# Kernel optimization log

Measured on AMD Instinct MI355X. Metric: run time of the kernel, lower is better.

## Reference

```python
import jax, jax.numpy as jnp
import numpy as np

N_NODES = 50000
N_EDGES = 800000
D_IN = 128
HIDDEN = 128
NUM_GRAPHS = 64
NUM_CLASSES = 6


def setup_inputs() -> dict:
    key = jax.random.key(0)
    ks = jax.random.split(key, 12)
    x = jax.random.normal(ks[0], (N_NODES, D_IN), dtype=jnp.float32)
    edge_index = jax.random.randint(ks[1], (2, N_EDGES), 0, N_NODES, dtype=jnp.int64)
    batch = jnp.sort(jax.random.randint(ks[2], (N_NODES,), 0, NUM_GRAPHS, dtype=jnp.int64))
    def glorot(k, fan_in, fan_out):
        s = jnp.sqrt(6.0 / (fan_in + fan_out)).astype(jnp.float32)
        return jax.random.uniform(k, (fan_in, fan_out), jnp.float32, -s, s)
    W0 = glorot(ks[3], D_IN, HIDDEN)
    b0 = jnp.zeros((HIDDEN,), jnp.float32)
    W1 = glorot(ks[4], HIDDEN, HIDDEN)
    b1 = jnp.zeros((HIDDEN,), jnp.float32)
    W2 = glorot(ks[5], HIDDEN, HIDDEN)
    b2 = jnp.zeros((HIDDEN,), jnp.float32)
    lin_W = glorot(ks[6], HIDDEN, NUM_CLASSES)
    lin_b = jnp.zeros((NUM_CLASSES,), jnp.float32)
    return {"x": x, "edge_index": edge_index, "batch": batch,
            "W0": W0, "b0": b0, "W1": W1, "b1": b1, "W2": W2, "b2": b2,
            "lin_W": lin_W, "lin_b": lin_b}


def reference(x, edge_index, batch, W0, b0, W1, b1, W2, b2, lin_W, lin_b):
    # GCNConv (PyG default): add self-loops, symmetric degree norm,
    # out = scatter_add(norm * (xW)[src] -> dst) + bias, then ReLU.
    loop = jnp.arange(N_NODES, dtype=edge_index.dtype)
    src = jnp.concatenate([edge_index[0], loop])  # message sources (x_j)
    dst = jnp.concatenate([edge_index[1], loop])  # aggregation targets
    deg = jax.ops.segment_sum(jnp.ones_like(dst, x.dtype), dst, num_segments=N_NODES)
    dinv = jnp.where(deg > 0, jax.lax.rsqrt(deg), 0.0)
    norm = (dinv[src] * dinv[dst])[:, None]  # [E+N, 1]

    h = x
    for W, b in ((W0, b0), (W1, b1), (W2, b2)):
        hw = h @ W                                   # [N, H] dense projection
        agg = jax.ops.segment_sum(hw[src] * norm, dst, num_segments=N_NODES)
        h = jax.nn.relu(agg + b)

    # global_mean_pool over graph ids
    counts = jax.ops.segment_sum(jnp.ones((N_NODES,), x.dtype), batch, num_segments=NUM_GRAPHS)
    embedding = jax.ops.segment_sum(h, batch, num_segments=NUM_GRAPHS) / jnp.maximum(counts, 1.0)[:, None]
    # dropout is identity in eval mode
    logits = embedding @ lin_W + lin_b
    return logits, embedding
```

## Files before the change

kernel.cpp:

```cpp
#include <hip/hip_runtime.h>

#define N_NODES 50000
#define HIDDEN 128
#define NUM_GRAPHS 64
#define NUM_CLASSES 6
#define SLOT_SHIFT 6
#define NB 782
#define NPAD 50048
#define ZROW 50040
#define BUCKET_CAP 1536
#define P1_CHUNK 2048
#define CONV_BLOCKS 96
#define LSTR 136

typedef __attribute__((ext_vector_type(8))) short short8;
typedef __attribute__((ext_vector_type(4))) float float4v;
typedef __attribute__((ext_vector_type(2))) float float2v;

__device__ __forceinline__ unsigned short f2b(float f) {
    unsigned u = __float_as_uint(f);
    return (unsigned short)((u + 0x7FFFu + ((u >> 16) & 1u)) >> 16);
}
__device__ __forceinline__ unsigned char f2e4m3(float f) {
    return (unsigned char)(__builtin_amdgcn_cvt_pk_fp8_f32(f, f, 0, false) & 0xFF);
}

__global__ __launch_bounds__(512) void pass1(const float* __restrict__ W0, const float* __restrict__ W1,
                                             const float* __restrict__ W2, unsigned short* __restrict__ wb,
                                             const int* __restrict__ src, const int* __restrict__ dst,
                                             int* __restrict__ gcursor, unsigned* __restrict__ ebuf, int e) {
    if (blockIdx.x < CONV_BLOCKS) {
        int i = blockIdx.x * 512 + threadIdx.x;
        int wsel = i >> 14;
        int r = i & 16383;
        int j = r & 7;
        int lane = (r >> 3) & 63;
        int f = r >> 9;
        int ki = f >> 3, nt = f & 7;
        int k = ki * 32 + (lane >> 4) * 8 + j;
        int c = nt * 16 + (lane & 15);
        const float* W = (wsel == 0) ? W0 : ((wsel == 1) ? W1 : W2);
        wb[i] = f2b(W[k * 128 + c]);
        return;
    }
    __shared__ unsigned hist[NB];
    __shared__ unsigned base[NB];
    const int t = threadIdx.x;
    const int start = (blockIdx.x - CONV_BLOCKS) * P1_CHUNK;
    for (int i = t; i < NB; i += 512) hist[i] = 0;
    __syncthreads();
    int lb[4];
    unsigned pk[4], lr[4];
    const int i0 = start + t * 4;
    int4 d4, s4;
    const bool full = (i0 + 3 < e);
    if (full) {
        d4 = *(const int4*)&dst[i0];
        s4 = *(const int4*)&src[i0];
    }
#pragma unroll
    for (int k = 0; k < 4; k++) {
        int i = i0 + k;
        lb[k] = -1;
        if (i < e) {
            int d = full ? ((const int*)&d4)[k] : dst[i];
            int s = full ? ((const int*)&s4)[k] : src[i];
            lb[k] = d >> 6;
            pk[k] = ((unsigned)(d & 63) << 16) | (unsigned)s;
            lr[k] = atomicAdd(&hist[lb[k]], 1u);
        }
    }
    __syncthreads();
    for (int b = t; b < NB; b += 512) {
        unsigned h = hist[b];
        base[b] = h ? (unsigned)atomicAdd(&gcursor[b], (int)h) : 0u;
    }
    __syncthreads();
#pragma unroll
    for (int k = 0; k < 4; k++) {
        if (lb[k] >= 0) {
            unsigned pos = base[lb[k]] + lr[k];
            if (pos < BUCKET_CAP) ebuf[lb[k] * BUCKET_CAP + pos] = pk[k];
        }
    }
}

__global__ __launch_bounds__(512) void pass2(const unsigned* __restrict__ ebuf, const int* __restrict__ gcursor,
                                             const float* __restrict__ x,
                                             unsigned short* __restrict__ csr16, int* __restrict__ cntc,
                                             float* __restrict__ dinv, unsigned char* __restrict__ xs8,
                                             unsigned char* __restrict__ h8a, unsigned char* __restrict__ h8b,
                                             int n) {
    __shared__ unsigned short csr_lds[64 * 64];
    __shared__ unsigned cnt[64];
    const int b = blockIdx.x;
    const int t = threadIdx.x;
    {
        const unsigned zz = ((unsigned)ZROW) | (((unsigned)ZROW) << 16);
        unsigned* cl = (unsigned*)csr_lds;
#pragma unroll
        for (int it = 0; it < 4; it++) cl[it * 512 + t] = zz;
    }
    if (t < 64) cnt[t] = 0;
    __syncthreads();
    if (t < 64) csr_lds[t * 64] = (unsigned short)(b * 64 + t);
    __syncthreads();
    const int nb = min(gcursor[b], BUCKET_CAP);
    {
        const int e0 = t * 4;
        if (e0 < nb) {
            uint4 e4 = *(const uint4*)&ebuf[b * BUCKET_CAP + e0];
            const int c4 = min(nb - e0, 4);
            const unsigned ev[4] = {e4.x, e4.y, e4.z, e4.w};
#pragma unroll
            for (int k = 0; k < 4; k++) {
                if (k < c4) {
                    unsigned e = ev[k];
                    int dl = (int)(e >> 16);
                    unsigned r = atomicAdd(&cnt[dl], 1u);
                    if (r < 63) csr_lds[dl * 64 + 1 + r] = (unsigned short)(e & 0xFFFFu);
                }
            }
        }
    }
    __syncthreads();
    {
        const unsigned* cu = (const unsigned*)csr_lds;
        unsigned* gout = (unsigned*)(csr16 + (size_t)b * 4096);
#pragma unroll
        for (int it = 0; it < 4; it++) gout[it * 512 + t] = cu[it * 512 + t];
    }
    if (t < 64) {
        int node = b * 64 + t;
        if (node < n) {
            int deg1 = (int)cnt[t] + 1;
            cntc[node] = min(deg1, 64);
            dinv[node] = rsqrtf((float)deg1);
        }
    }
#pragma unroll
    for (int it = 0; it < 4; it++) {
        int idx = it * 512 + t;
        int nl = idx >> 5;
        int el = (idx & 31) * 4;
        int gnode = b * 64 + nl;
        if (gnode < n) {
            float sc = rsqrtf((float)((int)cnt[nl] + 1));
            float4 v = *(const float4*)&x[gnode * 128 + el];
            unsigned lo = __builtin_amdgcn_cvt_pk_fp8_f32(v.x * sc, v.y * sc, 0, false);
            unsigned pkd = __builtin_amdgcn_cvt_pk_fp8_f32(v.z * sc, v.w * sc, lo, true);
            *(unsigned*)&xs8[gnode * 128 + el] = pkd;
        }
    }
    if (b == 0 && t < 384) {
        uint4 z = {0, 0, 0, 0};
        ((uint4*)(xs8 + (size_t)N_NODES * 128))[t] = z;
        ((uint4*)(h8a + (size_t)N_NODES * 128))[t] = z;
        ((uint4*)(h8b + (size_t)N_NODES * 128))[t] = z;
    }
}

template <bool LAST>
__global__ __launch_bounds__(256) void fused_layer(const unsigned char* __restrict__ hs8,
                                                   const int* __restrict__ cntc,
                                                   const unsigned short* __restrict__ csr16,
                                                   const float* __restrict__ dinv,
                                                   const unsigned short* __restrict__ wb,
                                                   const float* __restrict__ bias,
                                                   unsigned char* __restrict__ hout8,
                                                   const int* __restrict__ batchp,
                                                   float* __restrict__ embp) {
    __shared__ __align__(16) unsigned short tlds[16 * LSTR];
    __shared__ int bsh[16];
    const int wave = threadIdx.x >> 6;
    const int lane = threadIdx.x & 63;
    const int grp = lane >> 4;
    const int fl = lane & 15;
    const int node0 = blockIdx.x * 16;
    const int base_node = node0 + wave * 4;

    int nbv[4], mycv[4];
#pragma unroll
    for (int i = 0; i < 4; i++) nbv[i] = cntc[base_node + i];
#pragma unroll
    for (int i = 0; i < 4; i++)
        mycv[i] = (int)csr16[((base_node + i) << SLOT_SHIFT) + lane];

    for (int i = 0; i < 4; i++) {
        const int node = base_node + i;
        const int ng = (nbv[i] + 15) >> 4;
        const int myc = mycv[i];
        float2v a01 = {0.f, 0.f}, a23 = {0.f, 0.f}, a45 = {0.f, 0.f}, a67 = {0.f, 0.f};

        for (int g4 = 0; g4 < ng; g4++) {
            const int base = g4 << 4;
            int cc[4];
#pragma unroll
            for (int k = 0; k < 4; k++) cc[k] = __shfl(myc, base + k * 4 + grp, 64);
            uint2 u[4];
#pragma unroll
            for (int k = 0; k < 4; k++) u[k] = *(const uint2*)&hs8[cc[k] * 128 + fl * 8];
#pragma unroll
            for (int k = 0; k < 4; k++) {
                a01 += __builtin_amdgcn_cvt_pk_f32_fp8(u[k].x, false);
                a23 += __builtin_amdgcn_cvt_pk_f32_fp8(u[k].x, true);
                a45 += __builtin_amdgcn_cvt_pk_f32_fp8(u[k].y, false);
                a67 += __builtin_amdgcn_cvt_pk_f32_fp8(u[k].y, true);
            }
        }

        float acc[8] = {a01.x, a01.y, a23.x, a23.y, a45.x, a45.y, a67.x, a67.y};
#pragma unroll
        for (int j = 0; j < 8; j++) {
            acc[j] += __shfl_xor(acc[j], 16, 64);
            acc[j] += __shfl_xor(acc[j], 32, 64);
        }
        if (grp == 0) {
            const float dv = dinv[node];
            short8 o;
#pragma unroll
            for (int j = 0; j < 8; j++) o[j] = (short)f2b(acc[j] * dv);
            *(short8*)&tlds[(wave * 4 + i) * LSTR + fl * 8] = o;
        }
    }

    const int m = fl;
    const int quad = grp;
    const int nt0 = wave * 2;
    float bv[2];
#pragma unroll
    for (int q = 0; q < 2; q++) bv[q] = bias[(nt0 + q) * 16 + m];
    float sc[4];
    if (!LAST) {
#pragma unroll
        for (int reg = 0; reg < 4; reg++) sc[reg] = dinv[node0 + quad * 4 + reg];
    }
    if (LAST && threadIdx.x < 16) bsh[threadIdx.x] = batchp[node0 + threadIdx.x];
    __syncthreads();

    const short* B = (const short*)wb;
    float4v acc2[2];
    acc2[0] = (float4v){0.f, 0.f, 0.f, 0.f};
    acc2[1] = (float4v){0.f, 0.f, 0.f, 0.f};
#pragma unroll
    for (int ki = 0; ki < 4; ki++) {
        short8 a = *(const short8*)&tlds[m * LSTR + ki * 32 + quad * 8];
#pragma unroll
        for (int q = 0; q < 2; q++) {
            short8 b = *(const short8*)&B[((ki * 8 + nt0 + q) * 64 + lane) * 8];
            acc2[q] = __builtin_amdgcn_mfma_f32_16x16x32_bf16(a, b, acc2[q], 0, 0, 0);
        }
    }

    if (!LAST) {
#pragma unroll
        for (int q = 0; q < 2; q++) {
            int c = (nt0 + q) * 16 + m;
#pragma unroll
            for (int reg = 0; reg < 4; reg++) {
                int row = node0 + quad * 4 + reg;
                float v = fmaxf(acc2[q][reg] + bv[q], 0.f) * sc[reg];
                hout8[row * 128 + c] = f2e4m3(v);
            }
        }
    } else {
        const int g0 = bsh[0], g15 = bsh[15];
#pragma unroll
        for (int q = 0; q < 2; q++) {
            int c = (nt0 + q) * 16 + m;
            float v0 = fmaxf(acc2[q][0] + bv[q], 0.f);
            float v1 = fmaxf(acc2[q][1] + bv[q], 0.f);
            float v2 = fmaxf(acc2[q][2] + bv[q], 0.f);
            float v3 = fmaxf(acc2[q][3] + bv[q], 0.f);
            if (g0 == g15) {
                float s = v0 + v1 + v2 + v3;
                s += __shfl_xor(s, 16, 64);
                s += __shfl_xor(s, 32, 64);
                if (quad == 0) atomicAdd(&embp[g0 * HIDDEN + c], s);
            } else {
                for (int gg = g0; gg <= g15; ++gg) {
                    float s = (bsh[quad * 4 + 0] == gg ? v0 : 0.f)
                            + (bsh[quad * 4 + 1] == gg ? v1 : 0.f)
                            + (bsh[quad * 4 + 2] == gg ? v2 : 0.f)
                            + (bsh[quad * 4 + 3] == gg ? v3 : 0.f);
                    s += __shfl_xor(s, 16, 64);
                    s += __shfl_xor(s, 32, 64);
                    if (quad == 0) atomicAdd(&embp[gg * HIDDEN + c], s);
                }
            }
        }
    }
}

__global__ __launch_bounds__(128) void finalize_kernel(const float* __restrict__ emb,
                                                       const int* __restrict__ batch,
                                                       const float* __restrict__ linW, const float* __restrict__ linb,
                                                       float* out, int n) {
    const int g = blockIdx.x;
    const int f = threadIdx.x;
    __shared__ float es[128];
    __shared__ int bnd[2];
    if (f < 2) {
        int target = g + f;
        int lo = 0, hi = n;
        while (lo < hi) {
            int mid = (lo + hi) >> 1;
            if (batch[mid] < target) lo = mid + 1; else hi = mid;
        }
        bnd[f] = lo;
    }
    __syncthreads();
    float c = (float)max(bnd[1] - bnd[0], 1);
    float e = emb[g * HIDDEN + f] / c;
    out[NUM_GRAPHS * NUM_CLASSES + g * HIDDEN + f] = e;
    es[f] = e;
    __syncthreads();
    if (f < NUM_CLASSES) {
        float s = linb[f];
        for (int k = 0; k < HIDDEN; k++) s += es[k] * linW[k * NUM_CLASSES + f];
        out[g * NUM_CLASSES + f] = s;
    }
}

extern "C" void kernel_launch(void* const* d_in, const int* in_sizes, int n_in,
                              void* d_out, int out_size, void* d_ws, size_t ws_size,
                              hipStream_t stream) {
    const float* x    = (const float*)d_in[0];
    const int*   ei   = (const int*)d_in[1];
    const int*   batch= (const int*)d_in[2];
    const float* W0   = (const float*)d_in[3];
    const float* b0   = (const float*)d_in[4];
    const float* W1   = (const float*)d_in[5];
    const float* b1   = (const float*)d_in[6];
    const float* W2   = (const float*)d_in[7];
    const float* b2   = (const float*)d_in[8];
    const float* linW = (const float*)d_in[9];
    const float* linb = (const float*)d_in[10];
    float* out = (float*)d_out;

    const int N = N_NODES;
    const int E = in_sizes[1] / 2;
    const int* srcp = ei;
    const int* dstp = ei + E;

    char* w = (char*)d_ws;
    size_t o = 0;
    auto alloc = [&](size_t bytes) { size_t r = o; o += (bytes + 255) & ~(size_t)255; return r; };
    int*            gcursor = (int*)           (w + alloc((size_t)NB * 4));
    float*          emb     = (float*)         (w + alloc((size_t)NUM_GRAPHS * HIDDEN * 4));
    size_t zero_bytes = o;
    unsigned*       ebuf    = (unsigned*)      (w + alloc((size_t)NB * BUCKET_CAP * 4));
    unsigned short* csr16   = (unsigned short*)(w + alloc((size_t)NB * 64 * 64 * 2));
    int*            cntc    = (int*)           (w + alloc((size_t)N * 4));
    float*          dinv    = (float*)         (w + alloc((size_t)N * 4));
    unsigned char*  xs8     = (unsigned char*) (w + alloc((size_t)NPAD * HIDDEN));
    unsigned char*  h8a     = (unsigned char*) (w + alloc((size_t)NPAD * HIDDEN));
    unsigned char*  h8b     = (unsigned char*) (w + alloc((size_t)NPAD * HIDDEN));
    unsigned short* wb      = (unsigned short*)(w + alloc((size_t)3 * 16384 * 2));

    hipMemsetAsync(d_ws, 0, zero_bytes, stream);

    const int p1_edge_blocks = (E + P1_CHUNK - 1) / P1_CHUNK;

    pass1<<<CONV_BLOCKS + p1_edge_blocks, 512, 0, stream>>>(W0, W1, W2, wb, srcp, dstp, gcursor, ebuf, E);
    pass2<<<NB, 512, 0, stream>>>(ebuf, gcursor, x, csr16, cntc, dinv, xs8, h8a, h8b, N);

    const int fuse_grid = N / 16;

    fused_layer<false><<<fuse_grid, 256, 0, stream>>>(xs8, cntc, csr16, dinv, wb + 0 * 16384, b0, h8a,
                                                      nullptr, nullptr);
    fused_layer<false><<<fuse_grid, 256, 0, stream>>>(h8a, cntc, csr16, dinv, wb + 1 * 16384, b1, h8b,
                                                      nullptr, nullptr);
    fused_layer<true><<<fuse_grid, 256, 0, stream>>>(h8b, cntc, csr16, dinv, wb + 2 * 16384, b2, nullptr,
                                                     batch, emb);

    finalize_kernel<<<NUM_GRAPHS, 128, 0, stream>>>(emb, batch, linW, linb, out, N);
}
```

Before: 192.4 us.

## Build padded CSR directly with global atomics, dropping bucket sort pass

Edges are scattered straight into per-node 64-slot CSR rows using per-node global atomic counters, removing the intermediate bucket buffer and the second sort pass. Source ids are XOR-encoded so the zeroed memset leaves empty slots pointing at the zero padding row. A simpler prep kernel then computes degrees, normalizes and quantizes x, and writes the self-loop slot. The trade-off is many random global atomics and a larger memset, and neighbor order within a row becomes nondeterministic.

```diff
diff --git a/kernel.cpp b/kernel.cpp
--- a/kernel.cpp
+++ b/kernel.cpp
@@ -5,10 +5,9 @@
 #define NUM_GRAPHS 64
 #define NUM_CLASSES 6
 #define SLOT_SHIFT 6
-#define NB 782
 #define NPAD 50048
 #define ZROW 50040
-#define BUCKET_CAP 1536
+#define K_ENC 0xC378
 #define P1_CHUNK 2048
 #define CONV_BLOCKS 96
 #define LSTR 136
@@ -28,7 +27,7 @@
 __global__ __launch_bounds__(512) void pass1(const float* __restrict__ W0, const float* __restrict__ W1,
                                              const float* __restrict__ W2, unsigned short* __restrict__ wb,
                                              const int* __restrict__ src, const int* __restrict__ dst,
-                                             int* __restrict__ gcursor, unsigned* __restrict__ ebuf, int e) {
+                                             int* __restrict__ cnta, unsigned short* __restrict__ csr16, int e) {
     if (blockIdx.x < CONV_BLOCKS) {
         int i = blockIdx.x * 512 + threadIdx.x;
         int wsel = i >> 14;
@@ -43,15 +42,8 @@
         wb[i] = f2b(W[k * 128 + c]);
         return;
     }
-    __shared__ unsigned hist[NB];
-    __shared__ unsigned base[NB];
     const int t = threadIdx.x;
-    const int start = (blockIdx.x - CONV_BLOCKS) * P1_CHUNK;
-    for (int i = t; i < NB; i += 512) hist[i] = 0;
-    __syncthreads();
-    int lb[4];
-    unsigned pk[4], lr[4];
-    const int i0 = start + t * 4;
+    const int i0 = (blockIdx.x - CONV_BLOCKS) * P1_CHUNK + t * 4;
     int4 d4, s4;
     const bool full = (i0 + 3 < e);
     if (full) {
@@ -61,102 +53,38 @@
 #pragma unroll
     for (int k = 0; k < 4; k++) {
         int i = i0 + k;
-        lb[k] = -1;
         if (i < e) {
             int d = full ? ((const int*)&d4)[k] : dst[i];
             int s = full ? ((const int*)&s4)[k] : src[i];
-            lb[k] = d >> 6;
-            pk[k] = ((unsigned)(d & 63) << 16) | (unsigned)s;
-            lr[k] = atomicAdd(&hist[lb[k]], 1u);
-        }
-    }
-    __syncthreads();
-    for (int b = t; b < NB; b += 512) {
-        unsigned h = hist[b];
-        base[b] = h ? (unsigned)atomicAdd(&gcursor[b], (int)h) : 0u;
-    }
-    __syncthreads();
-#pragma unroll
-    for (int k = 0; k < 4; k++) {
-        if (lb[k] >= 0) {
-            unsigned pos = base[lb[k]] + lr[k];
-            if (pos < BUCKET_CAP) ebuf[lb[k] * BUCKET_CAP + pos] = pk[k];
-        }
-    }
-}
-
-__global__ __launch_bounds__(512) void pass2(const unsigned* __restrict__ ebuf, const int* __restrict__ gcursor,
-                                             const float* __restrict__ x,
-                                             unsigned short* __restrict__ csr16, int* __restrict__ cntc,
-                                             float* __restrict__ dinv, unsigned char* __restrict__ xs8,
-                                             unsigned char* __restrict__ h8a, unsigned char* __restrict__ h8b,
-                                             int n) {
-    __shared__ unsigned short csr_lds[64 * 64];
-    __shared__ unsigned cnt[64];
-    const int b = blockIdx.x;
-    const int t = threadIdx.x;
-    {
-        const unsigned zz = ((unsigned)ZROW) | (((unsigned)ZROW) << 16);
-        unsigned* cl = (unsigned*)csr_lds;
-#pragma unroll
-        for (int it = 0; it < 4; it++) cl[it * 512 + t] = zz;
-    }
-    if (t < 64) cnt[t] = 0;
-    __syncthreads();
-    if (t < 64) csr_lds[t * 64] = (unsigned short)(b * 64 + t);
-    __syncthreads();
-    const int nb = min(gcursor[b], BUCKET_CAP);
-    {
-        const int e0 = t * 4;
-        if (e0 < nb) {
-            uint4 e4 = *(const uint4*)&ebuf[b * BUCKET_CAP + e0];
-            const int c4 = min(nb - e0, 4);
-            const unsigned ev[4] = {e4.x, e4.y, e4.z, e4.w};
-#pragma unroll
-            for (int k = 0; k < 4; k++) {
-                if (k < c4) {
-                    unsigned e = ev[k];
-                    int dl = (int)(e >> 16);
-                    unsigned r = atomicAdd(&cnt[dl], 1u);
-                    if (r < 63) csr_lds[dl * 64 + 1 + r] = (unsigned short)(e & 0xFFFFu);
-                }
-            }
-        }
-    }
-    __syncthreads();
-    {
-        const unsigned* cu = (const unsigned*)csr_lds;
-        unsigned* gout = (unsigned*)(csr16 + (size_t)b * 4096);
-#pragma unroll
-        for (int it = 0; it < 4; it++) gout[it * 512 + t] = cu[it * 512 + t];
-    }
-    if (t < 64) {
-        int node = b * 64 + t;
-        if (node < n) {
-            int deg1 = (int)cnt[t] + 1;
+            int r = atomicAdd(&cnta[d], 1);
+            if (r < 63) csr16[d * 64 + 1 + r] = (unsigned short)(s ^ K_ENC);
+        }
+    }
+}
+
+__global__ __launch_bounds__(256) void prep(const int* __restrict__ cnta, const float* __restrict__ x,
+                                            unsigned short* __restrict__ csr16, int* __restrict__ cntc,
+                                            float* __restrict__ dinv, unsigned char* __restrict__ xs8,
+                                            unsigned char* __restrict__ h8a, unsigned char* __restrict__ h8b) {
+    const int idx = blockIdx.x * 256 + threadIdx.x;
+    const int node = idx >> 5;
+    const int el = (idx & 31) * 4;
+    if (node < N_NODES) {
+        const int deg1 = cnta[node] + 1;
+        const float sc = rsqrtf((float)deg1);
+        float4 v = *(const float4*)&x[node * 128 + el];
+        unsigned lo = __builtin_amdgcn_cvt_pk_fp8_f32(v.x * sc, v.y * sc, 0, false);
+        unsigned pkd = __builtin_amdgcn_cvt_pk_fp8_f32(v.z * sc, v.w * sc, lo, true);
+        *(unsigned*)&xs8[node * 128 + el] = pkd;
+        if (el == 0) {
             cntc[node] = min(deg1, 64);
-            dinv[node] = rsqrtf((float)deg1);
-        }
-    }
-#pragma unroll
-    for (int it = 0; it < 4; it++) {
-        int idx = it * 512 + t;
-        int nl = idx >> 5;
-        int el = (idx & 31) * 4;
-        int gnode = b * 64 + nl;
-        if (gnode < n) {
-            float sc = rsqrtf((float)((int)cnt[nl] + 1));
-            float4 v = *(const float4*)&x[gnode * 128 + el];
-            unsigned lo = __builtin_amdgcn_cvt_pk_fp8_f32(v.x * sc, v.y * sc, 0, false);
-            unsigned pkd = __builtin_amdgcn_cvt_pk_fp8_f32(v.z * sc, v.w * sc, lo, true);
-            *(unsigned*)&xs8[gnode * 128 + el] = pkd;
-        }
-    }
-    if (b == 0 && t < 384) {
-        uint4 z = {0, 0, 0, 0};
-        ((uint4*)(xs8 + (size_t)N_NODES * 128))[t] = z;
-        ((uint4*)(h8a + (size_t)N_NODES * 128))[t] = z;
-        ((uint4*)(h8b + (size_t)N_NODES * 128))[t] = z;
+            dinv[node] = sc;
+            csr16[node * 64] = (unsigned short)(node ^ K_ENC);
+        }
+    } else {
+        *(unsigned*)&xs8[node * 128 + el] = 0u;
+        *(unsigned*)&h8a[node * 128 + el] = 0u;
+        *(unsigned*)&h8b[node * 128 + el] = 0u;
     }
 }
 
@@ -184,7 +112,7 @@
     for (int i = 0; i < 4; i++) nbv[i] = cntc[base_node + i];
 #pragma unroll
     for (int i = 0; i < 4; i++)
-        mycv[i] = (int)csr16[((base_node + i) << SLOT_SHIFT) + lane];
+        mycv[i] = ((int)csr16[((base_node + i) << SLOT_SHIFT) + lane]) ^ K_ENC;
 
     for (int i = 0; i < 4; i++) {
         const int node = base_node + i;
@@ -346,11 +274,10 @@
     char* w = (char*)d_ws;
     size_t o = 0;
     auto alloc = [&](size_t bytes) { size_t r = o; o += (bytes + 255) & ~(size_t)255; return r; };
-    int*            gcursor = (int*)           (w + alloc((size_t)NB * 4));
     float*          emb     = (float*)         (w + alloc((size_t)NUM_GRAPHS * HIDDEN * 4));
+    int*            cnta    = (int*)           (w + alloc((size_t)N * 4));
+    unsigned short* csr16   = (unsigned short*)(w + alloc((size_t)NPAD * 64 * 2));
     size_t zero_bytes = o;
-    unsigned*       ebuf    = (unsigned*)      (w + alloc((size_t)NB * BUCKET_CAP * 4));
-    unsigned short* csr16   = (unsigned short*)(w + alloc((size_t)NB * 64 * 64 * 2));
     int*            cntc    = (int*)           (w + alloc((size_t)N * 4));
     float*          dinv    = (float*)         (w + alloc((size_t)N * 4));
     unsigned char*  xs8     = (unsigned char*) (w + alloc((size_t)NPAD * HIDDEN));
@@ -362,8 +289,8 @@
 
     const int p1_edge_blocks = (E + P1_CHUNK - 1) / P1_CHUNK;
 
-    pass1<<<CONV_BLOCKS + p1_edge_blocks, 512, 0, stream>>>(W0, W1, W2, wb, srcp, dstp, gcursor, ebuf, E);
-    pass2<<<NB, 512, 0, stream>>>(ebuf, gcursor, x, csr16, cntc, dinv, xs8, h8a, h8b, N);
+    pass1<<<CONV_BLOCKS + p1_edge_blocks, 512, 0, stream>>>(W0, W1, W2, wb, srcp, dstp, cnta, csr16, E);
+    prep<<<(NPAD * 32) / 256, 256, 0, stream>>>(cnta, x, csr16, cntc, dinv, xs8, h8a, h8b);
 
     const int fuse_grid = N / 16;
 
```

New measurement: 229.7 us. +19.4%, slower.
